# Kernel tuning notes

Measured on AMD Instinct MI355X. Metric: run time of the kernel, lower is better.

Reference implementation:

```python
import jax, jax.numpy as jnp
import numpy as np

B, DIM, X, Y = 2, 256, 48, 48
HEADS, DIM_HEAD = 8, 64
DIM_INNER = HEADS * DIM_HEAD
MASK_SELF_VALUE = -100.0
EPS = 1e-12


def setup_inputs() -> dict:
    key = jax.random.key(0)
    k0, k1, k2, k3, k4 = jax.random.split(key, 5)
    return {
        "fmap": jax.random.normal(k0, (B, DIM, X, Y), dtype=jnp.float32),
        "gamma": jnp.ones((DIM,), dtype=jnp.float32),
        "w_qk": jax.random.normal(k1, (DIM_INNER, DIM), dtype=jnp.float32) * 0.02,
        "w_v": jax.random.normal(k2, (DIM_INNER, DIM), dtype=jnp.float32) * 0.02,
        "null_kv": jax.random.normal(k3, (2, HEADS, DIM_HEAD), dtype=jnp.float32),
        "w_out": jax.random.normal(k4, (DIM, DIM_INNER), dtype=jnp.float32) * 0.02,
    }


def _safe_sqrt(d2):
    # matches torch.cdist subgradient: zero grad at zero distance
    pos = d2 > 0
    return jnp.where(pos, jnp.sqrt(jnp.where(pos, d2, 1.0)), 0.0)


def reference(fmap, gamma, w_qk, w_v, null_kv, w_out):
    b, c, x, y = fmap.shape
    h, dh = HEADS, DIM_HEAD
    n = x * y
    scale = dh ** -0.5

    # ChannelRMSNorm: L2-normalize over channel dim, * sqrt(dim) * gamma
    l2 = jnp.sqrt(jnp.sum(fmap * fmap, axis=1, keepdims=True))
    normed = fmap / jnp.maximum(l2, EPS) * jnp.sqrt(jnp.float32(c)) * gamma[None, :, None, None]

    flat = normed.reshape(b, c, n)                       # b c n
    qk = jnp.einsum('oc,bcn->bon', w_qk, flat)           # b (h d) n
    v = jnp.einsum('oc,bcn->bon', w_v, flat)
    qk = qk.reshape(b, h, dh, n).transpose(0, 1, 3, 2)   # b h n d
    v = v.reshape(b, h, dh, n).transpose(0, 1, 3, 2)

    nk = jnp.broadcast_to(null_kv[0][None, :, None, :], (b, h, 1, dh))
    nv = jnp.broadcast_to(null_kv[1][None, :, None, :], (b, h, 1, dh))
    q = qk
    k = jnp.concatenate([nk, qk], axis=2)                # b h (n+1) d
    vv = jnp.concatenate([nv, v], axis=2)

    # -cdist(q, k, p=2) * scale via squared-distance expansion
    q2 = jnp.sum(q * q, axis=-1)[..., :, None]           # b h n 1
    k2 = jnp.sum(k * k, axis=-1)[..., None, :]           # b h 1 n+1
    cross = jnp.einsum('bhid,bhjd->bhij', q, k)          # b h n n+1
    d2 = jnp.maximum(q2 + k2 - 2.0 * cross, 0.0)
    sim = -_safe_sqrt(d2) * scale

    # mask self: eye(n) left-padded by one (null token never masked)
    self_mask = jnp.eye(n, n + 1, k=1, dtype=bool)
    sim = jnp.where(self_mask, MASK_SELF_VALUE, sim)

    attn = jax.nn.softmax(sim, axis=-1)
    out = jnp.einsum('bhij,bhjd->bhid', attn, vv)        # b h n d
    out = out.transpose(0, 1, 3, 2).reshape(b, h * dh, x, y)
    return jnp.einsum('oc,bcxy->boxy', w_out, out)
```

## Files before the change

kernel.cpp:

```cpp
#include <hip/hip_runtime.h>
#include <math.h>

#define NPOS 2304
#define CC   256
#define DI   512
#define NT   36
#define SCALE 0.125f
#define MASKV -100.0f
#define NEGSL2E (-0.18033688011112042f)

typedef __attribute__((ext_vector_type(8))) short bf16x8;
typedef __attribute__((ext_vector_type(4))) float f32x4;
typedef unsigned short u16;
typedef unsigned int u32;

__device__ inline u16 f2bf(float f) {
    union { float f; unsigned int u; } v; v.f = f;
    return (u16)((v.u + 0x7fffu + ((v.u >> 16) & 1u)) >> 16);
}
__device__ inline float bf2f(u16 h) { return __uint_as_float(((u32)h) << 16); }

__device__ inline bf16x8 ld_x8(const u16* p) {
    union { bf16x8 v; uint2 d[2]; } u;
    u.d[0] = *(const uint2*)(p + 0);
    u.d[1] = *(const uint2*)(p + 4);
    return u.v;
}

__global__ __launch_bounds__(256) void k_proj(const float* __restrict__ fmap,
                                              const float* __restrict__ gamma,
                                              const float* __restrict__ wqk,
                                              const float* __restrict__ wv,
                                              const float* __restrict__ wout,
                                              const float* __restrict__ null_kv,
                                              u16* __restrict__ qkh,
                                              u16* __restrict__ vt,
                                              float* __restrict__ sq,
                                              float* __restrict__ ndot,
                                              float* __restrict__ nk2b,
                                              u16* __restrict__ wo_hi,
                                              u16* __restrict__ wo_lo) {
    const int blk = blockIdx.x;
    if (blk >= 576) {
        const int idx = blk - 576;
#pragma unroll
        for (int it = 0; it < 2; ++it) {
            const int k = idx * 512 + (int)threadIdx.x + it * 256;
            if (k < 32768) {
                const float4 v = ((const float4*)wout)[k];
                ushort4 h4, l4;
                h4.x = f2bf(v.x); l4.x = f2bf(v.x - bf2f(h4.x));
                h4.y = f2bf(v.y); l4.y = f2bf(v.y - bf2f(h4.y));
                h4.z = f2bf(v.z); l4.z = f2bf(v.z - bf2f(h4.z));
                h4.w = f2bf(v.w); l4.w = f2bf(v.w - bf2f(h4.w));
                ((ushort4*)wo_hi)[k] = h4;
                ((ushort4*)wo_lo)[k] = l4;
            }
        }
        return;
    }
    const int xcd = blk & 7;
    const int r   = blk >> 3;
    const int bh  = xcd * 2 + (r & 1);
    const int b   = bh >> 3;
    const int oy  = bh & 7;
    const int n0  = (r >> 1) * 64;

    const int t  = threadIdx.x;
    const int w = t >> 6, lane = t & 63, mcol = lane & 15, quad = lane >> 4;
    const int tx = t & 63, ty = t >> 6;

    __shared__ u16 X[64][260];
    __shared__ float red[4][64];
    __shared__ float inv_s[64];
    __shared__ float gs[256];
    __shared__ float sqp[4][64], ndp[4][64];
    u16 (*Tt)[68] = (u16(*)[68])X;

    gs[t] = gamma[t];
    const float* fb = fmap + (size_t)b * CC * NPOS;
    float v64[64];
#pragma unroll
    for (int i = 0; i < 64; ++i)
        v64[i] = fb[(ty * 64 + i) * NPOS + n0 + tx];
    float s = 0.0f;
#pragma unroll
    for (int i = 0; i < 64; ++i) s += v64[i] * v64[i];
    red[ty][tx] = s;
    __syncthreads();
    if (t < 64) {
        const float tt = red[0][t] + red[1][t] + red[2][t] + red[3][t];
        inv_s[t] = 16.0f / fmaxf(sqrtf(tt), 1e-12f);
    }
    __syncthreads();
    const float iv = inv_s[tx];
#pragma unroll
    for (int i = 0; i < 64; i += 2) {
        const int c = ty * 64 + i;
        const float v0 = v64[i] * iv * gs[c];
        const float v1 = v64[i + 1] * iv * gs[c + 1];
        *(u32*)&X[tx][c] = (u32)f2bf(v0) | ((u32)f2bf(v1) << 16);
    }
    if (blk == 0 && t < 8) {
        float s2 = 0.0f;
#pragma unroll 8
        for (int d = 0; d < 64; ++d) { const float x = null_kv[t * 64 + d]; s2 += x * x; }
        nk2b[t] = s2;
    }
    __syncthreads();

    const size_t wroff = (size_t)(oy * 64 + w * 16 + mcol) * 256 + quad * 8;
    const float* wrq = wqk + wroff;
    const float* wrv = wv + wroff;

    f32x4 cq[4], cv[4];
#pragma unroll
    for (int nf = 0; nf < 4; ++nf) {
        cq[nf] = (f32x4){0.f, 0.f, 0.f, 0.f};
        cv[nf] = (f32x4){0.f, 0.f, 0.f, 0.f};
    }
#pragma unroll
    for (int kc = 0; kc < 8; ++kc) {
        const float4 qa = *(const float4*)&wrq[kc * 32];
        const float4 qb4 = *(const float4*)&wrq[kc * 32 + 4];
        const float4 va = *(const float4*)&wrv[kc * 32];
        const float4 vb4 = *(const float4*)&wrv[kc * 32 + 4];
        bf16x8 aq, av;
        aq[0] = f2bf(qa.x);  aq[1] = f2bf(qa.y);  aq[2] = f2bf(qa.z);  aq[3] = f2bf(qa.w);
        aq[4] = f2bf(qb4.x); aq[5] = f2bf(qb4.y); aq[6] = f2bf(qb4.z); aq[7] = f2bf(qb4.w);
        av[0] = f2bf(va.x);  av[1] = f2bf(va.y);  av[2] = f2bf(va.z);  av[3] = f2bf(va.w);
        av[4] = f2bf(vb4.x); av[5] = f2bf(vb4.y); av[6] = f2bf(vb4.z); av[7] = f2bf(vb4.w);
        bf16x8 xB[4];
#pragma unroll
        for (int nf = 0; nf < 4; ++nf)
            xB[nf] = ld_x8(&X[nf * 16 + mcol][kc * 32 + quad * 8]);
#pragma unroll
        for (int nf = 0; nf < 4; ++nf) {
            cq[nf] = __builtin_amdgcn_mfma_f32_16x16x32_bf16(aq, xB[nf], cq[nf], 0, 0, 0);
            cv[nf] = __builtin_amdgcn_mfma_f32_16x16x32_bf16(av, xB[nf], cv[nf], 0, 0, 0);
        }
    }
    __syncthreads();

    {
        const int h = oy;
        const float4 nk4 = *(const float4*)&null_kv[h * 64 + w * 16 + quad * 4];
        float sv[4], nd[4];
#pragma unroll
        for (int nf = 0; nf < 4; ++nf) {
            sv[nf] = cq[nf][0] * cq[nf][0] + cq[nf][1] * cq[nf][1] + cq[nf][2] * cq[nf][2] + cq[nf][3] * cq[nf][3];
            nd[nf] = cq[nf][0] * nk4.x + cq[nf][1] * nk4.y + cq[nf][2] * nk4.z + cq[nf][3] * nk4.w;
        }
#pragma unroll
        for (int mk = 16; mk <= 32; mk <<= 1)
#pragma unroll
            for (int nf = 0; nf < 4; ++nf) {
                sv[nf] += __shfl_xor(sv[nf], mk);
                nd[nf] += __shfl_xor(nd[nf], mk);
            }
        if (quad == 0) {
#pragma unroll
            for (int nf = 0; nf < 4; ++nf) {
                sqp[w][nf * 16 + mcol] = sv[nf];
                ndp[w][nf * 16 + mcol] = nd[nf];
            }
        }
#pragma unroll
        for (int nf = 0; nf < 4; ++nf) {
            ushort4 r4;
            r4.x = f2bf(cq[nf][0]); r4.y = f2bf(cq[nf][1]);
            r4.z = f2bf(cq[nf][2]); r4.w = f2bf(cq[nf][3]);
            *(ushort4*)&Tt[nf * 16 + mcol][w * 16 + quad * 4] = r4;
        }
        __syncthreads();
        {
            const int n = t >> 2, ds = (t & 3) * 16;
            const uint2 r0 = *(const uint2*)&Tt[n][ds + 0];
            const uint2 r1 = *(const uint2*)&Tt[n][ds + 4];
            const uint2 r2 = *(const uint2*)&Tt[n][ds + 8];
            const uint2 r3 = *(const uint2*)&Tt[n][ds + 12];
            u16* dst = qkh + (((size_t)bh) * NPOS + n0 + n) * 64 + ds;
            *(uint4*)&dst[0] = make_uint4(r0.x, r0.y, r1.x, r1.y);
            *(uint4*)&dst[8] = make_uint4(r2.x, r2.y, r3.x, r3.y);
        }
        if (t < 64) {
            sq  [((size_t)bh) * NPOS + n0 + t] = sqp[0][t] + sqp[1][t] + sqp[2][t] + sqp[3][t];
            ndot[((size_t)bh) * NPOS + n0 + t] = ndp[0][t] + ndp[1][t] + ndp[2][t] + ndp[3][t];
        }
    }
    __syncthreads();

    {
#pragma unroll
        for (int nf = 0; nf < 4; ++nf)
#pragma unroll
            for (int rr = 0; rr < 4; ++rr)
                Tt[w * 16 + quad * 4 + rr][nf * 16 + mcol] = f2bf(cv[nf][rr]);
        __syncthreads();
        {
            const int d = t >> 2, ks = t & 3;
            const uint2 a0 = *(const uint2*)&Tt[d][ks * 16 + 0];
            const uint2 a1 = *(const uint2*)&Tt[d][ks * 16 + 4];
            const uint2 a2 = *(const uint2*)&Tt[d][ks * 16 + 8];
            const uint2 a3 = *(const uint2*)&Tt[d][ks * 16 + 12];
            u16* vdst = vt + (size_t)bh * (72 * 64 * 32);
            const int kb = (n0 >> 5) + (ks >> 1);
            u16* p = &vdst[((size_t)kb * 64 + d) * 32 + (ks & 1) * 16];
            *(uint4*)&p[0] = make_uint4(a0.x, a0.y, a1.x, a1.y);
            *(uint4*)&p[8] = make_uint4(a2.x, a2.y, a3.x, a3.y);
        }
    }
}

__global__ __launch_bounds__(256) void k_attn(const u16* __restrict__ qkh,
                                              const u16* __restrict__ vt,
                                              const float* __restrict__ null_kv,
                                              const float* __restrict__ nk2b,
                                              const float* __restrict__ sq,
                                              const float* __restrict__ ndot,
                                              u16* __restrict__ ih,
                                              u16* __restrict__ il) {
    const int blk = blockIdx.x;
    const int xcd = blk & 7;
    const int j = blk >> 3;
    const int bh = xcd * 2 + (j & 1);
    const int qb = j >> 1;
    const int q32 = qb * 32;
    const int tile0 = qb * 2;
    const int b = bh >> 3, h = bh & 7;
    const int t = threadIdx.x;
    const int wave = t >> 6, lane = t & 63;
    const int mcol = lane & 15, quad = lane >> 4;

    __shared__ __align__(16) char smem[18432];
    u16 (*Pt)[72] = (u16(*)[72])(smem + wave * 4608);

    const u16* qbase = qkh + (size_t)bh * NPOS * 64;
    const u16* vbase = vt + (size_t)bh * (72 * 64 * 32);
    const float* sqb = sq + (size_t)bh * NPOS;

    bf16x8 bq00, bq01, bq10, bq11;
    bq00 = *(const bf16x8*)&qbase[(q32 + mcol) * 64 + quad * 8];
    bq01 = *(const bf16x8*)&qbase[(q32 + mcol) * 64 + 32 + quad * 8];
    bq10 = *(const bf16x8*)&qbase[(q32 + 16 + mcol) * 64 + quad * 8];
    bq11 = *(const bf16x8*)&qbase[(q32 + 16 + mcol) * 64 + 32 + quad * 8];
    const float q2g0 = sqb[q32 + mcol];
    const float q2g1 = sqb[q32 + 16 + mcol];

    const bf16x8 ones = {0x3F80, 0x3F80, 0x3F80, 0x3F80, 0x3F80, 0x3F80, 0x3F80, 0x3F80};

    f32x4 oacc[2][4];
#pragma unroll
    for (int g = 0; g < 2; ++g)
#pragma unroll
        for (int nb = 0; nb < 4; ++nb) oacc[g][nb] = (f32x4){0.f, 0.f, 0.f, 0.f};
    f32x4 lsum0 = (f32x4){0.f, 0.f, 0.f, 0.f};
    f32x4 lsum1 = (f32x4){0.f, 0.f, 0.f, 0.f};

    const int kt0 = wave * 9;
#pragma unroll 2
    for (int k9 = 0; k9 < 9; ++k9) {
        const int kt = kt0 + k9;
        const int kj0 = kt * 64;

        bf16x8 bk[4][2], bv[4][2];
#pragma unroll
        for (int nb = 0; nb < 4; ++nb) {
            const u16* kr = &qbase[(kj0 + nb * 16 + mcol) * 64 + quad * 8];
            bk[nb][0] = *(const bf16x8*)&kr[0];
            bk[nb][1] = *(const bf16x8*)&kr[32];
        }
#pragma unroll
        for (int nb = 0; nb < 4; ++nb) {
            bv[nb][0] = *(const bf16x8*)&vbase[((size_t)(kt * 2 + 0) * 64 + nb * 16 + mcol) * 32 + quad * 8];
            bv[nb][1] = *(const bf16x8*)&vbase[((size_t)(kt * 2 + 1) * 64 + nb * 16 + mcol) * 32 + quad * 8];
        }
        float4 k2q[4];
#pragma unroll
        for (int nb = 0; nb < 4; ++nb)
            k2q[nb] = *(const float4*)&sqb[kj0 + nb * 16 + quad * 4];

        f32x4 c[2][4];
#pragma unroll
        for (int nb = 0; nb < 4; ++nb) {
            c[0][nb] = (f32x4){0.f, 0.f, 0.f, 0.f};
            c[0][nb] = __builtin_amdgcn_mfma_f32_16x16x32_bf16(bk[nb][0], bq00, c[0][nb], 0, 0, 0);
            c[0][nb] = __builtin_amdgcn_mfma_f32_16x16x32_bf16(bk[nb][1], bq01, c[0][nb], 0, 0, 0);
            c[1][nb] = (f32x4){0.f, 0.f, 0.f, 0.f};
            c[1][nb] = __builtin_amdgcn_mfma_f32_16x16x32_bf16(bk[nb][0], bq10, c[1][nb], 0, 0, 0);
            c[1][nb] = __builtin_amdgcn_mfma_f32_16x16x32_bf16(bk[nb][1], bq11, c[1][nb], 0, 0, 0);
        }

#pragma unroll
        for (int g = 0; g < 2; ++g) {
            const float q2 = g ? q2g1 : q2g0;
            const int ktm = (tile0 + g) >> 2, nbm = (tile0 + g) & 3;
#pragma unroll
            for (int nb = 0; nb < 4; ++nb) {
                float e[4];
#pragma unroll
                for (int r = 0; r < 4; ++r) {
                    const float pre = q2 + ((const float*)&k2q[nb])[r];
                    const float d2 = fmaxf(__builtin_fmaf(c[g][nb][r], -2.0f, pre), 0.0f);
                    e[r] = __builtin_amdgcn_exp2f(NEGSL2E * __builtin_amdgcn_sqrtf(d2));
                }
                if (kt == ktm && nb == nbm) {
#pragma unroll
                    for (int r = 0; r < 4; ++r)
                        if (quad * 4 + r == mcol) e[r] = 0.0f;
                }
                const u32 p01 = __builtin_amdgcn_perm(__float_as_uint(e[1]), __float_as_uint(e[0]), 0x07060302u);
                const u32 p23 = __builtin_amdgcn_perm(__float_as_uint(e[3]), __float_as_uint(e[2]), 0x07060302u);
                *(uint2*)&Pt[g * 16 + mcol][nb * 16 + quad * 4] = make_uint2(p01, p23);
            }
        }

        const bf16x8 bp00 = *(const bf16x8*)&Pt[mcol][quad * 8];
        const bf16x8 bp01 = *(const bf16x8*)&Pt[mcol][32 + quad * 8];
        const bf16x8 bp10 = *(const bf16x8*)&Pt[16 + mcol][quad * 8];
        const bf16x8 bp11 = *(const bf16x8*)&Pt[16 + mcol][32 + quad * 8];

#pragma unroll
        for (int nb = 0; nb < 4; ++nb) {
            oacc[0][nb] = __builtin_amdgcn_mfma_f32_16x16x32_bf16(bv[nb][0], bp00, oacc[0][nb], 0, 0, 0);
            oacc[0][nb] = __builtin_amdgcn_mfma_f32_16x16x32_bf16(bv[nb][1], bp01, oacc[0][nb], 0, 0, 0);
            oacc[1][nb] = __builtin_amdgcn_mfma_f32_16x16x32_bf16(bv[nb][0], bp10, oacc[1][nb], 0, 0, 0);
            oacc[1][nb] = __builtin_amdgcn_mfma_f32_16x16x32_bf16(bv[nb][1], bp11, oacc[1][nb], 0, 0, 0);
        }
        lsum0 = __builtin_amdgcn_mfma_f32_16x16x32_bf16(ones, bp00, lsum0, 0, 0, 0);
        lsum0 = __builtin_amdgcn_mfma_f32_16x16x32_bf16(ones, bp01, lsum0, 0, 0, 0);
        lsum1 = __builtin_amdgcn_mfma_f32_16x16x32_bf16(ones, bp10, lsum1, 0, 0, 0);
        lsum1 = __builtin_amdgcn_mfma_f32_16x16x32_bf16(ones, bp11, lsum1, 0, 0, 0);
    }

    float* Of = (float*)smem;
    float* Ow = Of + wave * (16 * 66);
#pragma unroll
    for (int p = 0; p < 2; ++p) {
        __syncthreads();
#pragma unroll
        for (int nb = 0; nb < 4; ++nb)
#pragma unroll
            for (int r = 0; r < 4; ++r)
                Ow[mcol * 66 + nb * 16 + quad * 4 + r] = oacc[p][nb][r];
        if (quad == 0) Ow[mcol * 66 + 64] = p ? lsum1[0] : lsum0[0];
        __syncthreads();

        const int q = t >> 4;
        const int d0 = (t & 15) * 4;
        float o[4] = {0.f, 0.f, 0.f, 0.f};
        float l = 0.0f;
#pragma unroll
        for (int w = 0; w < 4; ++w) {
            const float* src = Of + w * (16 * 66) + q * 66;
            const float4 a = *(const float4*)&src[d0];
            o[0] += a.x; o[1] += a.y; o[2] += a.z; o[3] += a.w;
            l += src[64];
        }
        const int qg = q32 + p * 16 + q;
        const float q2v = sqb[qg];
        const float nd = ndot[(size_t)bh * NPOS + qg];
        const float nk2 = nk2b[h];
        const float d2n = fmaxf(q2v + nk2 - 2.0f * nd, 0.0f);
        const float beta = __expf(-sqrtf(d2n) * SCALE);
        const float ilv = 1.0f / (l + beta);

        const float4 nv4 = *(const float4*)&null_kv[DI + h * 64 + d0];
        float v[4];
        v[0] = (o[0] + beta * nv4.x) * ilv;
        v[1] = (o[1] + beta * nv4.y) * ilv;
        v[2] = (o[2] + beta * nv4.z) * ilv;
        v[3] = (o[3] + beta * nv4.w) * ilv;
        ushort4 hi4, lo4;
        hi4.x = f2bf(v[0]); lo4.x = f2bf(v[0] - bf2f(hi4.x));
        hi4.y = f2bf(v[1]); lo4.y = f2bf(v[1] - bf2f(hi4.y));
        hi4.z = f2bf(v[2]); lo4.z = f2bf(v[2] - bf2f(hi4.z));
        hi4.w = f2bf(v[3]); lo4.w = f2bf(v[3] - bf2f(hi4.w));
        const size_t ob = ((size_t)b * NPOS + qg) * DI + h * 64 + d0;
        *(ushort4*)&ih[ob] = hi4;
        *(ushort4*)&il[ob] = lo4;
    }
}

__global__ __launch_bounds__(256) void k_out(const u16* __restrict__ wo_hi,
                                             const u16* __restrict__ wo_lo,
                                             const u16* __restrict__ ih,
                                             const u16* __restrict__ il,
                                             float* __restrict__ out) {
    const int j0 = blockIdx.x * 32;
    const int c0 = blockIdx.y * 64;
    const int b  = blockIdx.z;
    const int t  = threadIdx.x;
    const int w = t >> 6, lane = t & 63, mcol = lane & 15, quad = lane >> 4;

    const u16* ah = wo_hi + (size_t)(c0 + w * 16 + mcol) * 512 + quad * 8;
    const u16* al = wo_lo + (size_t)(c0 + w * 16 + mcol) * 512 + quad * 8;
    const u16* xh = ih + ((size_t)b * NPOS + j0 + mcol) * 512 + quad * 8;
    const u16* xl = il + ((size_t)b * NPOS + j0 + mcol) * 512 + quad * 8;

    f32x4 c[2];
#pragma unroll
    for (int nf = 0; nf < 2; ++nf) c[nf] = (f32x4){0.f, 0.f, 0.f, 0.f};
#pragma unroll
    for (int kc = 0; kc < 16; ++kc) {
        const bf16x8 A  = *(const bf16x8*)&ah[kc * 32];
        const bf16x8 Al = *(const bf16x8*)&al[kc * 32];
        bf16x8 Bh[2], Bl[2];
#pragma unroll
        for (int nf = 0; nf < 2; ++nf) {
            Bh[nf] = *(const bf16x8*)&xh[(size_t)nf * 16 * 512 + kc * 32];
            Bl[nf] = *(const bf16x8*)&xl[(size_t)nf * 16 * 512 + kc * 32];
        }
#pragma unroll
        for (int nf = 0; nf < 2; ++nf) {
            c[nf] = __builtin_amdgcn_mfma_f32_16x16x32_bf16(A,  Bh[nf], c[nf], 0, 0, 0);
            c[nf] = __builtin_amdgcn_mfma_f32_16x16x32_bf16(A,  Bl[nf], c[nf], 0, 0, 0);
            c[nf] = __builtin_amdgcn_mfma_f32_16x16x32_bf16(Al, Bh[nf], c[nf], 0, 0, 0);
        }
    }
    float* ob = out + ((size_t)b * CC + c0 + w * 16) * NPOS + j0;
#pragma unroll
    for (int nf = 0; nf < 2; ++nf)
#pragma unroll
        for (int r = 0; r < 4; ++r)
            ob[(size_t)(quad * 4 + r) * NPOS + nf * 16 + mcol] = c[nf][r];
}

extern "C" void kernel_launch(void* const* d_in, const int* in_sizes, int n_in,
                              void* d_out, int out_size, void* d_ws, size_t ws_size,
                              hipStream_t stream) {
    const float* fmap    = (const float*)d_in[0];
    const float* gamma   = (const float*)d_in[1];
    const float* w_qk    = (const float*)d_in[2];
    const float* w_v     = (const float*)d_in[3];
    const float* null_kv = (const float*)d_in[4];
    const float* w_out   = (const float*)d_in[5];
    float* out = (float*)d_out;

    u16* ws16 = (u16*)d_ws;
    u16* qkh    = ws16;
    u16* vtb    = qkh + 2359296;
    u16* in_hi  = vtb + 2359296;
    u16* in_lo  = in_hi + 2359296;
    u16* wo_hi  = in_lo + 2359296;
    u16* wo_lo  = wo_hi + 131072;
    float* sqbuf = (float*)(wo_lo + 131072);
    float* ndbuf = sqbuf + 36864;
    float* nk2b  = ndbuf + 36864;

    hipLaunchKernelGGL(k_proj, dim3(648),       dim3(256), 0, stream,
                       fmap, gamma, w_qk, w_v, w_out, null_kv, qkh, vtb, sqbuf, ndbuf, nk2b, wo_hi, wo_lo);
    hipLaunchKernelGGL(k_attn, dim3(1152),      dim3(256), 0, stream,
                       qkh, vtb, null_kv, nk2b, sqbuf, ndbuf, in_hi, in_lo);
    hipLaunchKernelGGL(k_out,  dim3(72, 4, 2),  dim3(256), 0, stream,
                       wo_hi, wo_lo, in_hi, in_lo, out);
}
```

Baseline: 194.3 us.

## Split attention key range across six waves and cut per-wave register pressure

The attention kernel now runs 384 threads (six waves), each covering 6 key tiles instead of 9, and the final reduction sums six partial accumulators. The score computation is split into two sequential halves with 4-element accumulators, and V fragments are loaded just before the PV MFMAs instead of up front. This lowers live registers per wave to raise occupancy and spreads the sequential key loop over more waves. The cost is more LDS, a wider cross-wave reduction, and V load latency that is less hidden.

```diff
diff --git a/kernel.cpp b/kernel.cpp
--- a/kernel.cpp
+++ b/kernel.cpp
@@ -212,7 +212,7 @@
     }
 }
 
-__global__ __launch_bounds__(256) void k_attn(const u16* __restrict__ qkh,
+__global__ __launch_bounds__(384) void k_attn(const u16* __restrict__ qkh,
                                               const u16* __restrict__ vt,
                                               const float* __restrict__ null_kv,
                                               const float* __restrict__ nk2b,
@@ -232,7 +232,7 @@
     const int wave = t >> 6, lane = t & 63;
     const int mcol = lane & 15, quad = lane >> 4;
 
-    __shared__ __align__(16) char smem[18432];
+    __shared__ __align__(16) char smem[27648];
     u16 (*Pt)[72] = (u16(*)[72])(smem + wave * 4608);
 
     const u16* qbase = qkh + (size_t)bh * NPOS * 64;
@@ -257,51 +257,40 @@
     f32x4 lsum0 = (f32x4){0.f, 0.f, 0.f, 0.f};
     f32x4 lsum1 = (f32x4){0.f, 0.f, 0.f, 0.f};
 
-    const int kt0 = wave * 9;
+    const int kt0 = wave * 6;
 #pragma unroll 2
-    for (int k9 = 0; k9 < 9; ++k9) {
-        const int kt = kt0 + k9;
+    for (int k6 = 0; k6 < 6; ++k6) {
+        const int kt = kt0 + k6;
         const int kj0 = kt * 64;
 
-        bf16x8 bk[4][2], bv[4][2];
+        bf16x8 bk[4][2];
 #pragma unroll
         for (int nb = 0; nb < 4; ++nb) {
             const u16* kr = &qbase[(kj0 + nb * 16 + mcol) * 64 + quad * 8];
             bk[nb][0] = *(const bf16x8*)&kr[0];
             bk[nb][1] = *(const bf16x8*)&kr[32];
         }
-#pragma unroll
-        for (int nb = 0; nb < 4; ++nb) {
-            bv[nb][0] = *(const bf16x8*)&vbase[((size_t)(kt * 2 + 0) * 64 + nb * 16 + mcol) * 32 + quad * 8];
-            bv[nb][1] = *(const bf16x8*)&vbase[((size_t)(kt * 2 + 1) * 64 + nb * 16 + mcol) * 32 + quad * 8];
-        }
         float4 k2q[4];
 #pragma unroll
         for (int nb = 0; nb < 4; ++nb)
             k2q[nb] = *(const float4*)&sqb[kj0 + nb * 16 + quad * 4];
 
-        f32x4 c[2][4];
-#pragma unroll
-        for (int nb = 0; nb < 4; ++nb) {
-            c[0][nb] = (f32x4){0.f, 0.f, 0.f, 0.f};
-            c[0][nb] = __builtin_amdgcn_mfma_f32_16x16x32_bf16(bk[nb][0], bq00, c[0][nb], 0, 0, 0);
-            c[0][nb] = __builtin_amdgcn_mfma_f32_16x16x32_bf16(bk[nb][1], bq01, c[0][nb], 0, 0, 0);
-            c[1][nb] = (f32x4){0.f, 0.f, 0.f, 0.f};
-            c[1][nb] = __builtin_amdgcn_mfma_f32_16x16x32_bf16(bk[nb][0], bq10, c[1][nb], 0, 0, 0);
-            c[1][nb] = __builtin_amdgcn_mfma_f32_16x16x32_bf16(bk[nb][1], bq11, c[1][nb], 0, 0, 0);
-        }
-
-#pragma unroll
-        for (int g = 0; g < 2; ++g) {
-            const float q2 = g ? q2g1 : q2g0;
-            const int ktm = (tile0 + g) >> 2, nbm = (tile0 + g) & 3;
+        {
+            f32x4 c[4];
+#pragma unroll
+            for (int nb = 0; nb < 4; ++nb) {
+                c[nb] = (f32x4){0.f, 0.f, 0.f, 0.f};
+                c[nb] = __builtin_amdgcn_mfma_f32_16x16x32_bf16(bk[nb][0], bq00, c[nb], 0, 0, 0);
+                c[nb] = __builtin_amdgcn_mfma_f32_16x16x32_bf16(bk[nb][1], bq01, c[nb], 0, 0, 0);
+            }
+            const int ktm = tile0 >> 2, nbm = tile0 & 3;
 #pragma unroll
             for (int nb = 0; nb < 4; ++nb) {
                 float e[4];
 #pragma unroll
                 for (int r = 0; r < 4; ++r) {
-                    const float pre = q2 + ((const float*)&k2q[nb])[r];
-                    const float d2 = fmaxf(__builtin_fmaf(c[g][nb][r], -2.0f, pre), 0.0f);
+                    const float pre = q2g0 + ((const float*)&k2q[nb])[r];
+                    const float d2 = fmaxf(__builtin_fmaf(c[nb][r], -2.0f, pre), 0.0f);
                     e[r] = __builtin_amdgcn_exp2f(NEGSL2E * __builtin_amdgcn_sqrtf(d2));
                 }
                 if (kt == ktm && nb == nbm) {
@@ -311,7 +300,35 @@
                 }
                 const u32 p01 = __builtin_amdgcn_perm(__float_as_uint(e[1]), __float_as_uint(e[0]), 0x07060302u);
                 const u32 p23 = __builtin_amdgcn_perm(__float_as_uint(e[3]), __float_as_uint(e[2]), 0x07060302u);
-                *(uint2*)&Pt[g * 16 + mcol][nb * 16 + quad * 4] = make_uint2(p01, p23);
+                *(uint2*)&Pt[mcol][nb * 16 + quad * 4] = make_uint2(p01, p23);
+            }
+        }
+        {
+            f32x4 c[4];
+#pragma unroll
+            for (int nb = 0; nb < 4; ++nb) {
+                c[nb] = (f32x4){0.f, 0.f, 0.f, 0.f};
+                c[nb] = __builtin_amdgcn_mfma_f32_16x16x32_bf16(bk[nb][0], bq10, c[nb], 0, 0, 0);
+                c[nb] = __builtin_amdgcn_mfma_f32_16x16x32_bf16(bk[nb][1], bq11, c[nb], 0, 0, 0);
+            }
+            const int ktm = (tile0 + 1) >> 2, nbm = (tile0 + 1) & 3;
+#pragma unroll
+            for (int nb = 0; nb < 4; ++nb) {
+                float e[4];
+#pragma unroll
+                for (int r = 0; r < 4; ++r) {
+                    const float pre = q2g1 + ((const float*)&k2q[nb])[r];
+                    const float d2 = fmaxf(__builtin_fmaf(c[nb][r], -2.0f, pre), 0.0f);
+                    e[r] = __builtin_amdgcn_exp2f(NEGSL2E * __builtin_amdgcn_sqrtf(d2));
+                }
+                if (kt == ktm && nb == nbm) {
+#pragma unroll
+                    for (int r = 0; r < 4; ++r)
+                        if (quad * 4 + r == mcol) e[r] = 0.0f;
+                }
+                const u32 p01 = __builtin_amdgcn_perm(__float_as_uint(e[1]), __float_as_uint(e[0]), 0x07060302u);
+                const u32 p23 = __builtin_amdgcn_perm(__float_as_uint(e[3]), __float_as_uint(e[2]), 0x07060302u);
+                *(uint2*)&Pt[16 + mcol][nb * 16 + quad * 4] = make_uint2(p01, p23);
             }
         }
 
@@ -319,13 +336,14 @@
         const bf16x8 bp01 = *(const bf16x8*)&Pt[mcol][32 + quad * 8];
         const bf16x8 bp10 = *(const bf16x8*)&Pt[16 + mcol][quad * 8];
         const bf16x8 bp11 = *(const bf16x8*)&Pt[16 + mcol][32 + quad * 8];
-
 #pragma unroll
         for (int nb = 0; nb < 4; ++nb) {
-            oacc[0][nb] = __builtin_amdgcn_mfma_f32_16x16x32_bf16(bv[nb][0], bp00, oacc[0][nb], 0, 0, 0);
-            oacc[0][nb] = __builtin_amdgcn_mfma_f32_16x16x32_bf16(bv[nb][1], bp01, oacc[0][nb], 0, 0, 0);
-            oacc[1][nb] = __builtin_amdgcn_mfma_f32_16x16x32_bf16(bv[nb][0], bp10, oacc[1][nb], 0, 0, 0);
-            oacc[1][nb] = __builtin_amdgcn_mfma_f32_16x16x32_bf16(bv[nb][1], bp11, oacc[1][nb], 0, 0, 0);
+            const bf16x8 bv0 = *(const bf16x8*)&vbase[((size_t)(kt * 2 + 0) * 64 + nb * 16 + mcol) * 32 + quad * 8];
+            const bf16x8 bv1 = *(const bf16x8*)&vbase[((size_t)(kt * 2 + 1) * 64 + nb * 16 + mcol) * 32 + quad * 8];
+            oacc[0][nb] = __builtin_amdgcn_mfma_f32_16x16x32_bf16(bv0, bp00, oacc[0][nb], 0, 0, 0);
+            oacc[0][nb] = __builtin_amdgcn_mfma_f32_16x16x32_bf16(bv1, bp01, oacc[0][nb], 0, 0, 0);
+            oacc[1][nb] = __builtin_amdgcn_mfma_f32_16x16x32_bf16(bv0, bp10, oacc[1][nb], 0, 0, 0);
+            oacc[1][nb] = __builtin_amdgcn_mfma_f32_16x16x32_bf16(bv1, bp11, oacc[1][nb], 0, 0, 0);
         }
         lsum0 = __builtin_amdgcn_mfma_f32_16x16x32_bf16(ones, bp00, lsum0, 0, 0, 0);
         lsum0 = __builtin_amdgcn_mfma_f32_16x16x32_bf16(ones, bp01, lsum0, 0, 0, 0);
@@ -346,39 +364,41 @@
         if (quad == 0) Ow[mcol * 66 + 64] = p ? lsum1[0] : lsum0[0];
         __syncthreads();
 
-        const int q = t >> 4;
-        const int d0 = (t & 15) * 4;
-        float o[4] = {0.f, 0.f, 0.f, 0.f};
-        float l = 0.0f;
-#pragma unroll
-        for (int w = 0; w < 4; ++w) {
-            const float* src = Of + w * (16 * 66) + q * 66;
-            const float4 a = *(const float4*)&src[d0];
-            o[0] += a.x; o[1] += a.y; o[2] += a.z; o[3] += a.w;
-            l += src[64];
-        }
-        const int qg = q32 + p * 16 + q;
-        const float q2v = sqb[qg];
-        const float nd = ndot[(size_t)bh * NPOS + qg];
-        const float nk2 = nk2b[h];
-        const float d2n = fmaxf(q2v + nk2 - 2.0f * nd, 0.0f);
-        const float beta = __expf(-sqrtf(d2n) * SCALE);
-        const float ilv = 1.0f / (l + beta);
-
-        const float4 nv4 = *(const float4*)&null_kv[DI + h * 64 + d0];
-        float v[4];
-        v[0] = (o[0] + beta * nv4.x) * ilv;
-        v[1] = (o[1] + beta * nv4.y) * ilv;
-        v[2] = (o[2] + beta * nv4.z) * ilv;
-        v[3] = (o[3] + beta * nv4.w) * ilv;
-        ushort4 hi4, lo4;
-        hi4.x = f2bf(v[0]); lo4.x = f2bf(v[0] - bf2f(hi4.x));
-        hi4.y = f2bf(v[1]); lo4.y = f2bf(v[1] - bf2f(hi4.y));
-        hi4.z = f2bf(v[2]); lo4.z = f2bf(v[2] - bf2f(hi4.z));
-        hi4.w = f2bf(v[3]); lo4.w = f2bf(v[3] - bf2f(hi4.w));
-        const size_t ob = ((size_t)b * NPOS + qg) * DI + h * 64 + d0;
-        *(ushort4*)&ih[ob] = hi4;
-        *(ushort4*)&il[ob] = lo4;
+        if (t < 256) {
+            const int q = t >> 4;
+            const int d0 = (t & 15) * 4;
+            float o[4] = {0.f, 0.f, 0.f, 0.f};
+            float l = 0.0f;
+#pragma unroll
+            for (int w = 0; w < 6; ++w) {
+                const float* src = Of + w * (16 * 66) + q * 66;
+                const float4 a = *(const float4*)&src[d0];
+                o[0] += a.x; o[1] += a.y; o[2] += a.z; o[3] += a.w;
+                l += src[64];
+            }
+            const int qg = q32 + p * 16 + q;
+            const float q2v = sqb[qg];
+            const float nd = ndot[(size_t)bh * NPOS + qg];
+            const float nk2 = nk2b[h];
+            const float d2n = fmaxf(q2v + nk2 - 2.0f * nd, 0.0f);
+            const float beta = __expf(-sqrtf(d2n) * SCALE);
+            const float ilv = 1.0f / (l + beta);
+
+            const float4 nv4 = *(const float4*)&null_kv[DI + h * 64 + d0];
+            float v[4];
+            v[0] = (o[0] + beta * nv4.x) * ilv;
+            v[1] = (o[1] + beta * nv4.y) * ilv;
+            v[2] = (o[2] + beta * nv4.z) * ilv;
+            v[3] = (o[3] + beta * nv4.w) * ilv;
+            ushort4 hi4, lo4;
+            hi4.x = f2bf(v[0]); lo4.x = f2bf(v[0] - bf2f(hi4.x));
+            hi4.y = f2bf(v[1]); lo4.y = f2bf(v[1] - bf2f(hi4.y));
+            hi4.z = f2bf(v[2]); lo4.z = f2bf(v[2] - bf2f(hi4.z));
+            hi4.w = f2bf(v[3]); lo4.w = f2bf(v[3] - bf2f(hi4.w));
+            const size_t ob = ((size_t)b * NPOS + qg) * DI + h * 64 + d0;
+            *(ushort4*)&ih[ob] = hi4;
+            *(ushort4*)&il[ob] = lo4;
+        }
     }
 }
 
@@ -450,7 +470,7 @@
 
     hipLaunchKernelGGL(k_proj, dim3(648),       dim3(256), 0, stream,
                        fmap, gamma, w_qk, w_v, w_out, null_kv, qkh, vtb, sqbuf, ndbuf, nk2b, wo_hi, wo_lo);
-    hipLaunchKernelGGL(k_attn, dim3(1152),      dim3(256), 0, stream,
+    hipLaunchKernelGGL(k_attn, dim3(1152),      dim3(384), 0, stream,
                        qkh, vtb, null_kv, nk2b, sqbuf, ndbuf, in_hi, in_lo);
     hipLaunchKernelGGL(k_out,  dim3(72, 4, 2),  dim3(256), 0, stream,
                        wo_hi, wo_lo, in_hi, in_lo, out);
```

New measurement: 207.6 us. +6.8%, slower.
